# Kernel optimization log

Measured on AMD Instinct MI355X. Metric: run time of the kernel, lower is better.

## Reference

```python
import jax, jax.numpy as jnp
import numpy as np

N = 30000      # nodes
E = 400000     # edges per sparse set / GAT graph
F_IN = 512     # num_features
NHID = 128     # nhid
H = 4          # GAT heads
NCLS = 10      # num_classes
NSETS = 5      # num_gat = (3**2-1)//2 + 1
EPS = 1e-5     # BatchNorm eps


def setup_inputs() -> dict:
    key = jax.random.key(0)
    ks = jax.random.split(key, 24)
    s_in = 1.0 / np.sqrt(F_IN)
    s_h = 1.0 / np.sqrt(NHID)
    s_hh = 1.0 / np.sqrt(H * NHID)
    inp = {
        "x": jax.random.normal(ks[0], (N, F_IN), jnp.float32),
        "edge_index": jax.random.randint(ks[1], (2, E), 0, N),
        "scatter_idx": jax.random.randint(ks[2], (NSETS, 2, E), 0, N),
        "scatter_w": jax.random.normal(ks[3], (NSETS, E), jnp.float32) * 0.1,
        "lin_in_W": jax.random.normal(ks[4], (F_IN, NHID), jnp.float32) * s_in,
        "lin_in_b": jnp.zeros((NHID,), jnp.float32),
        "gat_W": jax.random.normal(ks[5], (NSETS, NHID, H * NHID), jnp.float32) * s_h,
        "att_src": jax.random.normal(ks[6], (NSETS, H, NHID), jnp.float32) * s_h,
        "att_dst": jax.random.normal(ks[7], (NSETS, H, NHID), jnp.float32) * s_h,
        "gat_b": jnp.zeros((NSETS, H * NHID), jnp.float32),
        "mlp_W": jax.random.normal(ks[8], (NSETS, H * NHID, NHID), jnp.float32) * s_hh,
        "mlp_b": jnp.zeros((NSETS, NHID), jnp.float32),
        "bn_g": jnp.ones((NSETS, NHID), jnp.float32),
        "bn_b": jnp.zeros((NSETS, NHID), jnp.float32),
        "bn_m": jax.random.normal(ks[9], (NSETS, NHID), jnp.float32) * 0.1,
        "bn_v": jax.random.uniform(ks[10], (NSETS, NHID), jnp.float32) + 0.5,
        "bn0_g": jnp.ones((NHID,), jnp.float32),
        "bn0_b": jnp.zeros((NHID,), jnp.float32),
        "bn0_m": jax.random.normal(ks[11], (NHID,), jnp.float32) * 0.1,
        "bn0_v": jax.random.uniform(ks[12], (NHID,), jnp.float32) + 0.5,
        "out_W": jax.random.normal(ks[13], (NHID, NCLS), jnp.float32) * s_h,
        "out_b": jnp.zeros((NCLS,), jnp.float32),
    }
    return inp


def _forward(x, edge_index, scatter_idx, scatter_w, lin_in_W, lin_in_b,
             gat_W, att_src, att_dst, gat_b, mlp_W, mlp_b,
             bn_g, bn_b, bn_m, bn_v, bn0_g, bn0_b, bn0_m, bn0_v, out_W, out_b):
    # solo_pass: gather source features, weight by edge value, scatter-add at dest
    def sp(i, xx):
        msg = scatter_w[i][:, None] * xx[scatter_idx[i, 0]]          # [E, NHID]
        return jax.ops.segment_sum(msg, scatter_idx[i, 1], num_segments=N)

    h = x @ lin_in_W + lin_in_b                                       # [N, NHID]
    x0 = sp(0, h)
    xhs = [jnp.abs(sp(i, h)) for i in range(1, NSETS)]
    xs = [x0] + [sp(0, xh) for xh in xhs]

    # GATConv adds self-loops by default
    loops = jnp.arange(N)
    src = jnp.concatenate([edge_index[0], loops])
    dst = jnp.concatenate([edge_index[1], loops])

    def gat(i, xx):
        hh = (xx @ gat_W[i]).reshape(N, H, NHID)                      # [N,H,C]
        a_s = (hh * att_src[i]).sum(-1)                               # [N,H]
        a_d = (hh * att_dst[i]).sum(-1)                               # [N,H]
        e = jax.nn.leaky_relu(a_s[src] + a_d[dst], 0.2)               # [E+N,H]
        m = jax.ops.segment_max(e, dst, num_segments=N)
        ex = jnp.exp(e - m[dst])
        den = jax.ops.segment_sum(ex, dst, num_segments=N)
        alpha = ex / (den[dst] + 1e-16)                               # [E+N,H]
        out = jax.ops.segment_sum(alpha[:, :, None] * hh[src], dst, num_segments=N)
        return out.reshape(N, H * NHID) + gat_b[i]

    # Seq(ELU, Dropout(eval=no-op), Linear, BatchNorm1d(eval))
    def mlp(i, xx):
        z = jax.nn.elu(xx) @ mlp_W[i] + mlp_b[i]
        return (z - bn_m[i]) * jax.lax.rsqrt(bn_v[i] + EPS) * bn_g[i] + bn_b[i]

    outs = [mlp(i, gat(i, xs[i])) for i in range(NSETS)]
    x_stage2 = h + outs[0] + outs[1] + outs[2] + outs[3] + outs[4]

    z = (x_stage2 - bn0_m) * jax.lax.rsqrt(bn0_v + EPS) * bn0_g + bn0_b
    z = jax.nn.elu(z) @ out_W + out_b
    return jax.nn.log_softmax(z, axis=1)


def reference(x, edge_index, scatter_idx, scatter_w, lin_in_W, lin_in_b,
              gat_W, att_src, att_dst, gat_b, mlp_W, mlp_b,
              bn_g, bn_b, bn_m, bn_v, bn0_g, bn0_b, bn0_m, bn0_v, out_W, out_b):
    return _forward(x, edge_index, scatter_idx, scatter_w, lin_in_W, lin_in_b,
                    gat_W, att_src, att_dst, gat_b, mlp_W, mlp_b,
                    bn_g, bn_b, bn_m, bn_v, bn0_g, bn0_b, bn0_m, bn0_v, out_W, out_b)
```

## Files before the change

### kernel.cpp

```cpp
#include <hip/hip_runtime.h>
#include <cstdint>
#include <cstddef>

#define NN 30000
#define NE 400000
#define EG (NE + NN)
#define NSETS 5
#define NCLS 10
#define BN_EPS 1e-5f

#define NBKT 118
#define CHUNK 4096
#define NWG_SET 98
#define NWG_GAT 105
#define NWGMAX 105
#define NBLK_BIN (5 * NWG_SET + NWG_GAT)
#define NBLK_SORT (6 * NBKT)

typedef __bf16 bf16x8 __attribute__((ext_vector_type(8)));
typedef float  f32x4  __attribute__((ext_vector_type(4)));

constexpr size_t alg(size_t x) { return (x + 255) & ~size_t(255); }
constexpr size_t OFF_U1    = 0;
constexpr size_t OFF_HB    = OFF_U1   + alg((size_t)5 * NN * 128 * 2);
constexpr size_t OFF_X2    = OFF_HB   + alg((size_t)NN * 128 * 2);
constexpr size_t OFF_AGG   = OFF_X2   + alg((size_t)NN * 128 * 4);
constexpr size_t OFF_GOUT  = OFF_AGG  + alg((size_t)NN * 512 * 2);
constexpr size_t OFF_WT    = OFF_GOUT + alg((size_t)NN * 512 * 2);
constexpr size_t OFF_WATT  = OFF_WT   + alg((size_t)11 * 65536 * 2);
constexpr size_t OFF_OFF6  = OFF_WATT + alg((size_t)5 * 2 * 4 * 128 * 4);
constexpr size_t OFF_SPP   = OFF_OFF6 + alg((size_t)6 * (NN + 1) * 4);
constexpr size_t OFF_GSRC  = OFF_SPP  + alg((size_t)NSETS * NE * 8);
constexpr size_t OFF_CNT   = OFF_GSRC + alg((size_t)EG * 4);
constexpr size_t OFF_AS5   = OFF_CNT  + alg((size_t)12 * NN * 4);
constexpr size_t OFF_AD5   = OFF_AS5  + alg((size_t)5 * NN * 4 * 4);
constexpr size_t WS_NEED   = OFF_AD5  + alg((size_t)5 * NN * 4 * 4);

__device__ __forceinline__ float lrelu02(float v) { return v > 0.f ? v : 0.2f * v; }
__device__ __forceinline__ float eluf(float v)    { return v > 0.f ? v : __expf(v) - 1.f; }
__device__ __forceinline__ float bf2f(unsigned u) {
    union { unsigned i; float f; } c; c.i = u << 16; return c.f;
}
__device__ __forceinline__ unsigned short f2bf(float f) {
    union { float f; unsigned i; } c; c.f = f;
    unsigned u = c.i + 0x7FFFu + ((c.i >> 16) & 1u);
    return (unsigned short)(u >> 16);
}
__device__ __forceinline__ void gload_lds16(const void* g, void* l) {
    __builtin_amdgcn_global_load_lds(
        (const __attribute__((address_space(1))) void*)(uintptr_t)g,
        (__attribute__((address_space(3))) void*)(unsigned)(uintptr_t)l,
        16, 0, 0);
}

__device__ __forceinline__ void chunk_map(int blk, int& g, int& wg, int& e0, int& e1) {
    if (blk < 5 * NWG_SET) { g = blk / NWG_SET; wg = blk - g * NWG_SET; }
    else                   { g = 5;             wg = blk - 5 * NWG_SET; }
    e0 = wg * CHUNK;
    e1 = min(e0 + CHUNK, (g < 5) ? NE : EG);
}

#define PREP_CVX_B 1024
#define PREP_TRW_B 512
#define PREP_WAT_B 20
#define PREP_HIST_B NBLK_BIN
#define PREP_GRID (PREP_CVX_B + PREP_TRW_B + PREP_WAT_B + PREP_HIST_B)

__global__ void prep1(const int* __restrict__ scat_idx, const int* __restrict__ edge_ix,
                      int* __restrict__ bh,
                      const float* __restrict__ x, unsigned short* __restrict__ xb,
                      const float* __restrict__ lin_W, const float* __restrict__ gat_W,
                      const float* __restrict__ mlp_W,
                      unsigned short* __restrict__ linWT, unsigned short* __restrict__ gatWT,
                      unsigned short* __restrict__ mlpWT,
                      const float* __restrict__ att_src, const float* __restrict__ att_dst,
                      float* __restrict__ watt) {
    __shared__ int h[NBKT];
    const int b = blockIdx.x;
    if (b < PREP_CVX_B) {
        const int total = NN * 512 / 4;
        for (int i = b * 256 + threadIdx.x; i < total; i += PREP_CVX_B * 256) {
            float4 v = *(const float4*)(x + (size_t)i * 4);
            ushort4 o;
            o.x = f2bf(v.x); o.y = f2bf(v.y); o.z = f2bf(v.z); o.w = f2bf(v.w);
            *(ushort4*)(xb + (size_t)i * 4) = o;
        }
    } else if (b < PREP_CVX_B + PREP_TRW_B) {
        const int bb = b - PREP_CVX_B;
        const int total = 65536 + 2 * 327680;
        for (int i = bb * 256 + threadIdx.x; i < total; i += PREP_TRW_B * 256) {
            if (i < 65536) {
                int n = i >> 9, k = i & 511;
                linWT[i] = f2bf(lin_W[(size_t)k * 128 + n]);
            } else if (i < 65536 + 327680) {
                int li = i - 65536;
                int st = li >> 16, r = li & 65535;
                int n = r >> 7, k = r & 127;
                gatWT[li] = f2bf(gat_W[(size_t)st * 65536 + (size_t)k * 512 + n]);
            } else {
                int li = i - 65536 - 327680;
                int st = li >> 16, r = li & 65535;
                int n = r >> 9, k = r & 511;
                mlpWT[li] = f2bf(mlp_W[(size_t)st * 65536 + (size_t)k * 128 + n]);
            }
        }
    } else if (b < PREP_CVX_B + PREP_TRW_B + PREP_WAT_B) {
        const int tid = (b - PREP_CVX_B - PREP_TRW_B) * 256 + threadIdx.x;
        if (tid < 5120) {
            int k = tid & 127, hh = (tid >> 7) & 3, tt = (tid >> 9) & 1, i = tid >> 10;
            const float* att = (tt == 0 ? att_src : att_dst) + ((size_t)i * 4 + hh) * 128;
            const float* Wr  = gat_W + ((size_t)i * 128 + k) * 512 + hh * 128;
            float s = 0.f;
            #pragma unroll 8
            for (int c = 0; c < 128; ++c) s = fmaf(Wr[c], att[c], s);
            watt[tid] = s;
        }
    } else {
        const int blk = b - (PREP_CVX_B + PREP_TRW_B + PREP_WAT_B);
        int g, wg, e0, e1;
        chunk_map(blk, g, wg, e0, e1);
        for (int i = threadIdx.x; i < NBKT; i += 256) h[i] = 0;
        __syncthreads();
        if (g < 5) {
            const int* dsts = scat_idx + (size_t)g * 2 * NE + NE;
            for (int e = e0 + threadIdx.x; e < e1; e += 256)
                atomicAdd(&h[dsts[e] >> 8], 1);
        } else {
            for (int e = e0 + threadIdx.x; e < e1; e += 256) {
                int d = (e < NE) ? edge_ix[NE + e] : (e - NE);
                atomicAdd(&h[d >> 8], 1);
            }
        }
        __syncthreads();
        for (int i = threadIdx.x; i < NBKT; i += 256)
            bh[(size_t)(g * NBKT + i) * NWGMAX + wg] = h[i];
    }
}

__global__ void bktscan(const int* __restrict__ bh, int* __restrict__ bb, int* __restrict__ off6) {
    const int g = blockIdx.x;
    const int t = threadIdx.x;
    const int nwg = (g < 5) ? NWG_SET : NWG_GAT;
    __shared__ int s[128];
    int tot = 0;
    if (t < NBKT) {
        const int* p = bh + (size_t)(g * NBKT + t) * NWGMAX;
        for (int w = 0; w < nwg; ++w) tot += p[w];
    }
    s[t] = tot;
    __syncthreads();
    for (int d = 1; d < 128; d <<= 1) {
        int u = (t >= d) ? s[t - d] : 0;
        __syncthreads();
        s[t] += u;
        __syncthreads();
    }
    if (t < NBKT) bb[g * 132 + t] = s[t] - tot;
    if (t == NBKT - 1) {
        bb[g * 132 + NBKT] = s[t];
        off6[g * (NN + 1) + NN] = s[t];
    }
}

__global__ void wgscan(const int* __restrict__ bb, int* __restrict__ bh) {
    const int gb = blockIdx.x;
    const int g = gb / NBKT, bk = gb - g * NBKT;
    __shared__ int s[128];
    const int t = threadIdx.x;
    const int nwg = (g < 5) ? NWG_SET : NWG_GAT;
    int v = (t < nwg) ? bh[(size_t)gb * NWGMAX + t] : 0;
    s[t] = v;
    __syncthreads();
    for (int d = 1; d < 128; d <<= 1) {
        int u = (t >= d) ? s[t - d] : 0;
        __syncthreads();
        s[t] += u;
        __syncthreads();
    }
    const int base = bb[g * 132 + bk];
    if (t < nwg) bh[(size_t)gb * NWGMAX + t] = base + (s[t] - v);
}

__global__ void __launch_bounds__(256) binP(const int* __restrict__ scat_idx, const float* __restrict__ scat_w,
                                            const int* __restrict__ edge_ix, const int* __restrict__ pos,
                                            int2* __restrict__ stg_sp, int* __restrict__ stg_g) {
    __shared__ int lpos[NBKT];
    __shared__ int lcur[NBKT];
    int g, wg, e0, e1;
    chunk_map(blockIdx.x, g, wg, e0, e1);
    for (int i = threadIdx.x; i < NBKT; i += 256) {
        lpos[i] = pos[(size_t)(g * NBKT + i) * NWGMAX + wg];
        lcur[i] = 0;
    }
    __syncthreads();
    if (g < 5) {
        const int* si = scat_idx + (size_t)g * 2 * NE;
        const float* sw = scat_w + (size_t)g * NE;
        for (int e = e0 + threadIdx.x; e < e1; e += 256) {
            int src = si[e], d = si[NE + e];
            int r = atomicAdd(&lcur[d >> 8], 1);
            int2 pk; pk.x = src | (d << 15); pk.y = __float_as_int(sw[e]);
            stg_sp[(size_t)g * NE + lpos[d >> 8] + r] = pk;
        }
    } else {
        for (int e = e0 + threadIdx.x; e < e1; e += 256) {
            int src, d;
            if (e < NE) { src = edge_ix[e]; d = edge_ix[NE + e]; }
            else        { src = e - NE;     d = src; }
            int r = atomicAdd(&lcur[d >> 8], 1);
            stg_g[lpos[d >> 8] + r] = src | (d << 15);
        }
    }
}

__global__ void __launch_bounds__(256) sortP(const int* __restrict__ bb,
                                             const int2* __restrict__ stg_sp, const int* __restrict__ stg_g,
                                             int2* __restrict__ spp, int* __restrict__ g_src,
                                             int* __restrict__ off6) {
    __shared__ int lcnt[256];
    __shared__ int loff[257];
    const int gb = blockIdx.x;
    const int g = gb / NBKT, bk = gb - g * NBKT;
    const int n0 = bk << 8;
    const int nlen = min(256, NN - n0);
    const int base = bb[g * 132 + bk];
    const int end  = bb[g * 132 + bk + 1];
    const int t = threadIdx.x;
    lcnt[t] = 0;
    __syncthreads();
    if (g < 5) {
        for (int j = base + t; j < end; j += 256)
            atomicAdd(&lcnt[((stg_sp[(size_t)g * NE + j].x >> 15) & 0x7fff) - n0], 1);
    } else {
        for (int j = base + t; j < end; j += 256)
            atomicAdd(&lcnt[((stg_g[j] >> 15) & 0x7fff) - n0], 1);
    }
    __syncthreads();
    int v = lcnt[t];
    __syncthreads();
    for (int d = 1; d < 256; d <<= 1) {
        int u = (t >= d) ? lcnt[t - d] : 0;
        __syncthreads();
        lcnt[t] += u;
        __syncthreads();
    }
    loff[t] = base + lcnt[t] - v;
    if (t == 255) loff[256] = base + lcnt[255];
    __syncthreads();
    if (t < nlen) off6[g * (NN + 1) + n0 + t] = loff[t];
    lcnt[t] = 0;
    __syncthreads();
    if (g < 5) {
        for (int j = base + t; j < end; j += 256) {
            int2 pk = stg_sp[(size_t)g * NE + j];
            int ln = ((pk.x >> 15) & 0x7fff) - n0;
            int p = loff[ln] + atomicAdd(&lcnt[ln], 1);
            int2 o; o.x = pk.x & 0x7fff; o.y = pk.y;
            spp[(size_t)g * NE + p] = o;
        }
    } else {
        for (int j = base + t; j < end; j += 256) {
            int w = stg_g[j];
            int ln = ((w >> 15) & 0x7fff) - n0;
            int p = loff[ln] + atomicAdd(&lcnt[ln], 1);
            g_src[p] = w & 0x7fff;
        }
    }
}

template<int ROWS>
__device__ __forceinline__ void stage64(const unsigned short* __restrict__ src, int ld,
                                        int row0, int maxrow, int k0, char* lds, int t) {
    const int wave = t >> 6, lane = t & 63;
    const int sub = lane >> 3;
    const int kch = (lane & 7) ^ sub;
    for (int j = wave; j < ROWS / 8; j += 4) {
        int grow = row0 + j * 8 + sub;
        if (grow > maxrow) grow = maxrow;
        gload_lds16(src + (size_t)grow * ld + k0 + kch * 8, lds + j * 1024);
    }
}

__global__ void __launch_bounds__(256) mgemm_lin(const unsigned short* __restrict__ A,
                                                 const unsigned short* __restrict__ BT,
                                                 const float* __restrict__ bias,
                                                 unsigned short* __restrict__ outb,
                                                 float* __restrict__ x2) {
    constexpr int K = 512, NC = 128;
    __shared__ __align__(16) char As[64 * 128];
    __shared__ __align__(16) char Bs[128 * 128];
    const int t = threadIdx.x, wave = t >> 6, lane = t & 63;
    const int bm = blockIdx.x * 64;
    const int wr = (wave >> 1) * 32, wc = (wave & 1) * 64;
    const int l15 = lane & 15, l4 = lane >> 4;
    const int rsw = (l15 & 7) << 4;
    f32x4 acc[2][4] = {};

    for (int kt = 0; kt < K; kt += 64) {
        stage64<64>(A, K, bm, NN - 1, kt, As, t);
        stage64<128>(BT, K, 0, NC - 1, kt, Bs, t);
        __syncthreads();
        #pragma unroll
        for (int kk = 0; kk < 2; ++kk) {
            bf16x8 af[2], bf[4];
            const int koff = kk * 64 + l4 * 16;
            #pragma unroll
            for (int fm = 0; fm < 2; ++fm)
                af[fm] = *(const bf16x8*)(As + (wr + fm * 16 + l15) * 128 + (koff ^ rsw));
            #pragma unroll
            for (int fn = 0; fn < 4; ++fn)
                bf[fn] = *(const bf16x8*)(Bs + (wc + fn * 16 + l15) * 128 + (koff ^ rsw));
            #pragma unroll
            for (int fm = 0; fm < 2; ++fm)
                #pragma unroll
                for (int fn = 0; fn < 4; ++fn)
                    acc[fm][fn] = __builtin_amdgcn_mfma_f32_16x16x32_bf16(af[fm], bf[fn], acc[fm][fn], 0, 0, 0);
        }
        __syncthreads();
    }

    #pragma unroll
    for (int fn = 0; fn < 4; ++fn) {
        const int c = wc + fn * 16 + l15;
        const float bias_c = bias[c];
        #pragma unroll
        for (int fm = 0; fm < 2; ++fm) {
            #pragma unroll
            for (int rg = 0; rg < 4; ++rg) {
                int r = bm + wr + fm * 16 + l4 * 4 + rg;
                if (r < NN) {
                    float v = acc[fm][fn][rg] + bias_c;
                    outb[(size_t)r * NC + c] = f2bf(v);
                    x2[(size_t)r * NC + c] = v;
                }
            }
        }
    }
}

__global__ void __launch_bounds__(256) fusedGM(const unsigned short* __restrict__ agg,
                                               const unsigned short* __restrict__ gatWT,
                                               const unsigned short* __restrict__ mlpWT,
                                               const float* __restrict__ gat_b,
                                               const float* __restrict__ mlp_b,
                                               const float* __restrict__ bng, const float* __restrict__ bnb,
                                               const float* __restrict__ bnm, const float* __restrict__ bnv,
                                               float* __restrict__ x2) {
    __shared__ __align__(16) char U[49152];
    __shared__ __align__(16) char gtile[16384];
    const int t = threadIdx.x, wave = t >> 6, lane = t & 63;
    const int bm = blockIdx.x * 64;
    const int wr = (wave >> 1) * 32, wc = (wave & 1) * 64;
    const int l15 = lane & 15, l4 = lane >> 4;
    const int rsw = (l15 & 7) << 4;
    f32x4 acc2[2][4] = {};

    #pragma unroll
    for (int h = 0; h < 4; ++h) {
        stage64<64>(agg, 512, bm, NN - 1, h * 128,       U,         t);
        stage64<64>(agg, 512, bm, NN - 1, h * 128 + 64,  U + 8192,  t);
        stage64<128>(gatWT, 128, h * 128, 511, 0,        U + 16384, t);
        stage64<128>(gatWT, 128, h * 128, 511, 64,       U + 32768, t);
        __syncthreads();

        f32x4 a1[2][4] = {};
        #pragma unroll
        for (int ks = 0; ks < 4; ++ks) {
            const char* Asb = U + (ks >> 1) * 8192;
            const char* Bsb = U + 16384 + (ks >> 1) * 16384;
            const int koff = (ks & 1) * 64 + l4 * 16;
            bf16x8 af[2], bf[4];
            #pragma unroll
            for (int fm = 0; fm < 2; ++fm)
                af[fm] = *(const bf16x8*)(Asb + (wr + fm * 16 + l15) * 128 + (koff ^ rsw));
            #pragma unroll
            for (int fn = 0; fn < 4; ++fn)
                bf[fn] = *(const bf16x8*)(Bsb + (wc + fn * 16 + l15) * 128 + (koff ^ rsw));
            #pragma unroll
            for (int fm = 0; fm < 2; ++fm)
                #pragma unroll
                for (int fn = 0; fn < 4; ++fn)
                    a1[fm][fn] = __builtin_amdgcn_mfma_f32_16x16x32_bf16(af[fm], bf[fn], a1[fm][fn], 0, 0, 0);
        }
        __syncthreads();

        #pragma unroll
        for (int fn = 0; fn < 4; ++fn) {
            const int cc = wc + fn * 16 + l15;
            const float gb = gat_b[h * 128 + cc];
            #pragma unroll
            for (int fm = 0; fm < 2; ++fm) {
                #pragma unroll
                for (int rg = 0; rg < 4; ++rg) {
                    const int r = wr + fm * 16 + l4 * 4 + rg;
                    const unsigned short v = f2bf(eluf(a1[fm][fn][rg] + gb));
                    *(unsigned short*)(gtile + r * 256 + ((((cc >> 3) ^ (r & 7)) << 4) | ((cc & 7) << 1))) = v;
                }
            }
        }
        stage64<128>(mlpWT, 512, 0, 127, h * 128,      U,         t);
        stage64<128>(mlpWT, 512, 0, 127, h * 128 + 64, U + 16384, t);
        __syncthreads();

        #pragma unroll
        for (int ks = 0; ks < 4; ++ks) {
            const int s2 = ks >> 1, kk = ks & 1;
            const char* slab = U + s2 * 16384;
            bf16x8 af[2], bf[4];
            #pragma unroll
            for (int fm = 0; fm < 2; ++fm) {
                const int r2 = wr + fm * 16 + l15;
                const int chunk = (s2 * 8 + kk * 4 + l4) ^ (r2 & 7);
                af[fm] = *(const bf16x8*)(gtile + r2 * 256 + (chunk << 4));
            }
            const int koff = kk * 64 + l4 * 16;
            #pragma unroll
            for (int fn = 0; fn < 4; ++fn)
                bf[fn] = *(const bf16x8*)(slab + (wc + fn * 16 + l15) * 128 + (koff ^ rsw));
            #pragma unroll
            for (int fm = 0; fm < 2; ++fm)
                #pragma unroll
                for (int fn = 0; fn < 4; ++fn)
                    acc2[fm][fn] = __builtin_amdgcn_mfma_f32_16x16x32_bf16(af[fm], bf[fn], acc2[fm][fn], 0, 0, 0);
        }
        __syncthreads();
    }

    #pragma unroll
    for (int fn = 0; fn < 4; ++fn) {
        const int c = wc + fn * 16 + l15;
        const float sc = bng[c] * rsqrtf(bnv[c] + BN_EPS);
        const float sh = bnb[c] - bnm[c] * sc;
        const float mb = mlp_b[c];
        #pragma unroll
        for (int fm = 0; fm < 2; ++fm) {
            #pragma unroll
            for (int rg = 0; rg < 4; ++rg) {
                int r = bm + wr + fm * 16 + l4 * 4 + rg;
                if (r < NN)
                    x2[(size_t)r * 128 + c] += (acc2[fm][fn][rg] + mb) * sc + sh;
            }
        }
    }
}

__global__ void __launch_bounds__(256) sp_abs_all(const int* __restrict__ off6,
                                                  const int2* __restrict__ spp,
                                                  const unsigned short* __restrict__ hb,
                                                  unsigned short* __restrict__ tmpI) {
    const int wid  = blockIdx.x * 4 + (threadIdx.x >> 6);
    const int lane = threadIdx.x & 63;
    const int co   = lane * 2;
    float a[4][2];
    #pragma unroll
    for (int y = 0; y < 4; ++y) {
        const int* off = off6 + (y + 1) * (NN + 1);
        const int2* pk = spp + (size_t)(y + 1) * NE;
        const int s0 = off[wid], s1 = off[wid + 1];
        float a0 = 0.f, a1 = 0.f;
        int j = s0;
        for (; j + 3 < s1; j += 4) {
            int2 e0 = pk[j], e1 = pk[j + 1], e2 = pk[j + 2], e3 = pk[j + 3];
            unsigned v0 = *(const unsigned*)(hb + (size_t)e0.x * 128 + co);
            unsigned v1 = *(const unsigned*)(hb + (size_t)e1.x * 128 + co);
            unsigned v2 = *(const unsigned*)(hb + (size_t)e2.x * 128 + co);
            unsigned v3 = *(const unsigned*)(hb + (size_t)e3.x * 128 + co);
            float w0 = __int_as_float(e0.y), w1 = __int_as_float(e1.y);
            float w2 = __int_as_float(e2.y), w3 = __int_as_float(e3.y);
            a0 = fmaf(w0, bf2f(v0 & 0xffffu), a0); a1 = fmaf(w0, bf2f(v0 >> 16), a1);
            a0 = fmaf(w1, bf2f(v1 & 0xffffu), a0); a1 = fmaf(w1, bf2f(v1 >> 16), a1);
            a0 = fmaf(w2, bf2f(v2 & 0xffffu), a0); a1 = fmaf(w2, bf2f(v2 >> 16), a1);
            a0 = fmaf(w3, bf2f(v3 & 0xffffu), a0); a1 = fmaf(w3, bf2f(v3 >> 16), a1);
        }
        for (; j < s1; ++j) {
            int2 e = pk[j];
            float wj = __int_as_float(e.y);
            unsigned v = *(const unsigned*)(hb + (size_t)e.x * 128 + co);
            a0 = fmaf(wj, bf2f(v & 0xffffu), a0);
            a1 = fmaf(wj, bf2f(v >> 16), a1);
        }
        a[y][0] = fabsf(a0);
        a[y][1] = fabsf(a1);
    }
    uint4 o;
    o.x = (unsigned)f2bf(a[0][0]) | ((unsigned)f2bf(a[1][0]) << 16);
    o.y = (unsigned)f2bf(a[2][0]) | ((unsigned)f2bf(a[3][0]) << 16);
    o.z = (unsigned)f2bf(a[0][1]) | ((unsigned)f2bf(a[1][1]) << 16);
    o.w = (unsigned)f2bf(a[2][1]) | ((unsigned)f2bf(a[3][1]) << 16);
    *(uint4*)(tmpI + (size_t)wid * 512 + co * 4) = o;
}

__global__ void __launch_bounds__(256) sp_fused5(const int* __restrict__ off0,
                                                 const int2* __restrict__ spp0,
                                                 const unsigned short* __restrict__ hb,
                                                 const unsigned short* __restrict__ tmpI,
                                                 unsigned short* __restrict__ xcur5,
                                                 const float* __restrict__ watt,
                                                 float* __restrict__ as5,
                                                 float* __restrict__ ad5) {
    __shared__ float sWatt[5120];
    for (int i = threadIdx.x; i < 5120; i += 256) sWatt[i] = watt[i];
    __syncthreads();

    const int wid  = blockIdx.x * 4 + (threadIdx.x >> 6);
    const int lane = threadIdx.x & 63;
    const int co   = lane * 2;
    const int s0 = off0[wid], s1 = off0[wid + 1];

    float a[5][2] = {};
    int j = s0;
    for (; j + 3 < s1; j += 4) {
        int2 e0 = spp0[j], e1 = spp0[j + 1], e2 = spp0[j + 2], e3 = spp0[j + 3];
        unsigned h0 = *(const unsigned*)(hb + (size_t)e0.x * 128 + co);
        unsigned h1 = *(const unsigned*)(hb + (size_t)e1.x * 128 + co);
        unsigned h2 = *(const unsigned*)(hb + (size_t)e2.x * 128 + co);
        unsigned h3 = *(const unsigned*)(hb + (size_t)e3.x * 128 + co);
        uint4 t0 = *(const uint4*)(tmpI + (size_t)e0.x * 512 + co * 4);
        uint4 t1 = *(const uint4*)(tmpI + (size_t)e1.x * 512 + co * 4);
        uint4 t2 = *(const uint4*)(tmpI + (size_t)e2.x * 512 + co * 4);
        uint4 t3 = *(const uint4*)(tmpI + (size_t)e3.x * 512 + co * 4);
        float w0 = __int_as_float(e0.y), w1 = __int_as_float(e1.y);
        float w2 = __int_as_float(e2.y), w3 = __int_as_float(e3.y);
        #define ACC1(W, H, T) \
            a[0][0] = fmaf(W, bf2f((H) & 0xffffu), a[0][0]); a[0][1] = fmaf(W, bf2f((H) >> 16), a[0][1]); \
            a[1][0] = fmaf(W, bf2f((T).x & 0xffffu), a[1][0]); a[2][0] = fmaf(W, bf2f((T).x >> 16), a[2][0]); \
            a[3][0] = fmaf(W, bf2f((T).y & 0xffffu), a[3][0]); a[4][0] = fmaf(W, bf2f((T).y >> 16), a[4][0]); \
            a[1][1] = fmaf(W, bf2f((T).z & 0xffffu), a[1][1]); a[2][1] = fmaf(W, bf2f((T).z >> 16), a[2][1]); \
            a[3][1] = fmaf(W, bf2f((T).w & 0xffffu), a[3][1]); a[4][1] = fmaf(W, bf2f((T).w >> 16), a[4][1]);
        ACC1(w0, h0, t0)
        ACC1(w1, h1, t1)
        ACC1(w2, h2, t2)
        ACC1(w3, h3, t3)
    }
    for (; j < s1; ++j) {
        int2 e = spp0[j];
        float wj = __int_as_float(e.y);
        unsigned hh = *(const unsigned*)(hb + (size_t)e.x * 128 + co);
        uint4 tt = *(const uint4*)(tmpI + (size_t)e.x * 512 + co * 4);
        ACC1(wj, hh, tt)
    }
    #undef ACC1
    #pragma unroll
    for (int y = 0; y < 5; ++y) {
        unsigned o = (unsigned)f2bf(a[y][0]) | ((unsigned)f2bf(a[y][1]) << 16);
        *(unsigned*)(xcur5 + (size_t)y * NN * 128 + (size_t)wid * 128 + co) = o;
    }

    #pragma unroll
    for (int i = 0; i < 5; ++i) {
        #pragma unroll
        for (int h = 0; h < 4; ++h) {
            const float* wS = sWatt + ((i * 2 + 0) * 4 + h) * 128;
            const float* wD = sWatt + ((i * 2 + 1) * 4 + h) * 128;
            float ps = a[i][0] * wS[co] + a[i][1] * wS[co + 1];
            float pd = a[i][0] * wD[co] + a[i][1] * wD[co + 1];
            #pragma unroll
            for (int dd = 1; dd < 64; dd <<= 1) { ps += __shfl_xor(ps, dd); pd += __shfl_xor(pd, dd); }
            if (lane == 0) {
                as5[(size_t)i * NN * 4 + (size_t)wid * 4 + h] = ps;
                ad5[(size_t)i * NN * 4 + (size_t)wid * 4 + h] = pd;
            }
        }
    }
}

__device__ __forceinline__ void acc8(float* a, float al, uint4 v) {
    a[0] = fmaf(al, bf2f(v.x & 0xffffu), a[0]); a[1] = fmaf(al, bf2f(v.x >> 16), a[1]);
    a[2] = fmaf(al, bf2f(v.y & 0xffffu), a[2]); a[3] = fmaf(al, bf2f(v.y >> 16), a[3]);
    a[4] = fmaf(al, bf2f(v.z & 0xffffu), a[4]); a[5] = fmaf(al, bf2f(v.z >> 16), a[5]);
    a[6] = fmaf(al, bf2f(v.w & 0xffffu), a[6]); a[7] = fmaf(al, bf2f(v.w >> 16), a[7]);
}

__global__ void __launch_bounds__(256) gat_agg2(const int* __restrict__ goff, const int* __restrict__ gsrc,
                                                const float* __restrict__ as_, const float* __restrict__ ad_,
                                                const unsigned short* __restrict__ xcur,
                                                unsigned short* __restrict__ agg) {
    const int wid  = blockIdx.x * 4 + (threadIdx.x >> 6);
    const int lane = threadIdx.x & 63;
    const int hd   = lane >> 4;
    const int cl   = (lane & 15) * 8;
    const int s0 = goff[wid], s1 = goff[wid + 1];
    const float4 adv4 = *(const float4*)(ad_ + (size_t)wid * 4);

    float m[4] = {-1e30f, -1e30f, -1e30f, -1e30f};
    float s[4] = {0.f, 0.f, 0.f, 0.f};
    for (int j = s0 + lane; j < s1; j += 64) {
        const int si = gsrc[j];
        float4 av = *(const float4*)(as_ + (size_t)si * 4);
        float e[4] = {lrelu02(av.x + adv4.x), lrelu02(av.y + adv4.y),
                      lrelu02(av.z + adv4.z), lrelu02(av.w + adv4.w)};
        #pragma unroll
        for (int h = 0; h < 4; ++h) {
            if (e[h] > m[h]) { s[h] = s[h] * __expf(m[h] - e[h]) + 1.f; m[h] = e[h]; }
            else             { s[h] += __expf(e[h] - m[h]); }
        }
    }
    #pragma unroll
    for (int d = 1; d < 64; d <<= 1) {
        #pragma unroll
        for (int h = 0; h < 4; ++h) {
            float om = __shfl_xor(m[h], d);
            float os = __shfl_xor(s[h], d);
            float nm = fmaxf(m[h], om);
            s[h] = s[h] * __expf(m[h] - nm) + os * __expf(om - nm);
            m[h] = nm;
        }
    }
    const float advh = hd == 0 ? adv4.x : hd == 1 ? adv4.y : hd == 2 ? adv4.z : adv4.w;
    const float mv   = hd == 0 ? m[0]   : hd == 1 ? m[1]   : hd == 2 ? m[2]   : m[3];
    const float dv   = hd == 0 ? s[0]   : hd == 1 ? s[1]   : hd == 2 ? s[2]   : s[3];
    const float inv  = 1.f / (dv + 1e-16f);

    float ac[8] = {};
    int j = s0;
    for (; j + 3 < s1; j += 4) {
        int i0 = gsrc[j], i1 = gsrc[j + 1], i2 = gsrc[j + 2], i3 = gsrc[j + 3];
        float q0 = as_[(size_t)i0 * 4 + hd], q1 = as_[(size_t)i1 * 4 + hd];
        float q2 = as_[(size_t)i2 * 4 + hd], q3 = as_[(size_t)i3 * 4 + hd];
        uint4 v0 = *(const uint4*)(xcur + (size_t)i0 * 128 + cl);
        uint4 v1 = *(const uint4*)(xcur + (size_t)i1 * 128 + cl);
        uint4 v2 = *(const uint4*)(xcur + (size_t)i2 * 128 + cl);
        uint4 v3 = *(const uint4*)(xcur + (size_t)i3 * 128 + cl);
        float al0 = __expf(lrelu02(q0 + advh) - mv) * inv;
        float al1 = __expf(lrelu02(q1 + advh) - mv) * inv;
        float al2 = __expf(lrelu02(q2 + advh) - mv) * inv;
        float al3 = __expf(lrelu02(q3 + advh) - mv) * inv;
        acc8(ac, al0, v0); acc8(ac, al1, v1); acc8(ac, al2, v2); acc8(ac, al3, v3);
    }
    for (; j < s1; ++j) {
        int si = gsrc[j];
        float q = as_[(size_t)si * 4 + hd];
        uint4 v = *(const uint4*)(xcur + (size_t)si * 128 + cl);
        float al = __expf(lrelu02(q + advh) - mv) * inv;
        acc8(ac, al, v);
    }
    uint4 ov;
    ov.x = (unsigned)f2bf(ac[0]) | ((unsigned)f2bf(ac[1]) << 16);
    ov.y = (unsigned)f2bf(ac[2]) | ((unsigned)f2bf(ac[3]) << 16);
    ov.z = (unsigned)f2bf(ac[4]) | ((unsigned)f2bf(ac[5]) << 16);
    ov.w = (unsigned)f2bf(ac[6]) | ((unsigned)f2bf(ac[7]) << 16);
    *(uint4*)(agg + (size_t)wid * 512 + hd * 128 + cl) = ov;
}

__global__ void __launch_bounds__(256) final_out(const float* __restrict__ x2,
                                                 const float* __restrict__ bn0g, const float* __restrict__ bn0b,
                                                 const float* __restrict__ bn0m, const float* __restrict__ bn0v,
                                                 const float* __restrict__ outW, const float* __restrict__ outb,
                                                 float* __restrict__ out) {
    __shared__ float sW[128 * 12];
    __shared__ float sSc[128], sSh[128];
    for (int i = threadIdx.x; i < 1280; i += 256) {
        int r = i / 10, c = i - r * 10;
        sW[r * 12 + c] = outW[i];
    }
    if (threadIdx.x < 128) {
        int c = threadIdx.x;
        float sc = bn0g[c] * rsqrtf(bn0v[c] + BN_EPS);
        sSc[c] = sc;
        sSh[c] = bn0b[c] - bn0m[c] * sc;
    }
    __syncthreads();
    const int wid  = blockIdx.x * 4 + (threadIdx.x >> 6);
    const int lane = threadIdx.x & 63;
    const int c0 = lane * 2;
    float2 a = *(const float2*)(x2 + (size_t)wid * 128 + c0);
    float a0 = eluf(a.x * sSc[c0] + sSh[c0]);
    float a1 = eluf(a.y * sSc[c0 + 1] + sSh[c0 + 1]);
    float p[NCLS];
    #pragma unroll
    for (int j = 0; j < NCLS; ++j)
        p[j] = a0 * sW[c0 * 12 + j] + a1 * sW[(c0 + 1) * 12 + j];
    #pragma unroll
    for (int j = 0; j < NCLS; ++j) {
        float v = p[j];
        v += __shfl_xor(v, 1);  v += __shfl_xor(v, 2);  v += __shfl_xor(v, 4);
        v += __shfl_xor(v, 8);  v += __shfl_xor(v, 16); v += __shfl_xor(v, 32);
        p[j] = v;
    }
    float z[NCLS];
    #pragma unroll
    for (int j = 0; j < NCLS; ++j) z[j] = p[j] + outb[j];
    float m = z[0];
    #pragma unroll
    for (int j = 1; j < NCLS; ++j) m = fmaxf(m, z[j]);
    float ssum = 0.f;
    #pragma unroll
    for (int j = 0; j < NCLS; ++j) ssum += __expf(z[j] - m);
    float lse = m + __logf(ssum);
    #pragma unroll
    for (int j = 0; j < NCLS; ++j)
        if (lane == j) out[(size_t)wid * NCLS + j] = z[j] - lse;
}

extern "C" void kernel_launch(void* const* d_in, const int* in_sizes, int n_in,
                              void* d_out, int out_size, void* d_ws, size_t ws_size,
                              hipStream_t stream) {
    const float* x        = (const float*)d_in[0];
    const int*   edge_ix  = (const int*)  d_in[1];
    const int*   scat_idx = (const int*)  d_in[2];
    const float* scat_w   = (const float*)d_in[3];
    const float* lin_W    = (const float*)d_in[4];
    const float* lin_b    = (const float*)d_in[5];
    const float* gat_W    = (const float*)d_in[6];
    const float* att_src  = (const float*)d_in[7];
    const float* att_dst  = (const float*)d_in[8];
    const float* gat_b    = (const float*)d_in[9];
    const float* mlp_W    = (const float*)d_in[10];
    const float* mlp_b    = (const float*)d_in[11];
    const float* bn_g     = (const float*)d_in[12];
    const float* bn_b     = (const float*)d_in[13];
    const float* bn_m     = (const float*)d_in[14];
    const float* bn_v     = (const float*)d_in[15];
    const float* bn0_g    = (const float*)d_in[16];
    const float* bn0_b    = (const float*)d_in[17];
    const float* bn0_m    = (const float*)d_in[18];
    const float* bn0_v    = (const float*)d_in[19];
    const float* out_W    = (const float*)d_in[20];
    const float* out_b    = (const float*)d_in[21];
    float* out = (float*)d_out;

    char* ws = (char*)d_ws;
    unsigned short* xb    = (unsigned short*)(ws + OFF_U1);
    unsigned short* xcur5 = (unsigned short*)(ws + OFF_U1);
    unsigned short* hb    = (unsigned short*)(ws + OFF_HB);
    float*          x2    = (float*)(ws + OFF_X2);
    unsigned short* agg   = (unsigned short*)(ws + OFF_AGG);
    unsigned short* tmpI  = (unsigned short*)(ws + OFF_GOUT);
    int2*  stg_sp = (int2*)(ws + OFF_GOUT);
    int*   stg_g  = (int*)(ws + OFF_GOUT + (size_t)NSETS * NE * 8);
    unsigned short* wt    = (unsigned short*)(ws + OFF_WT);
    unsigned short* linWT = wt;
    unsigned short* gatWT = wt + 65536;
    unsigned short* mlpWT = wt + 65536 * 6;
    float* watt   = (float*)(ws + OFF_WATT);
    int*   off6   = (int*)(ws + OFF_OFF6);
    int2*  spp    = (int2*)(ws + OFF_SPP);
    int*   g_src  = (int*)(ws + OFF_GSRC);
    int*   bh     = (int*)(ws + OFF_CNT);
    int*   bb     = bh + NBLK_SORT * NWGMAX;
    float* as5    = (float*)(ws + OFF_AS5);
    float* ad5    = (float*)(ws + OFF_AD5);

    const dim3 b256(256);

    prep1<<<PREP_GRID, b256, 0, stream>>>(scat_idx, edge_ix, bh, x, xb,
                                          lin_W, gat_W, mlp_W, linWT, gatWT, mlpWT,
                                          att_src, att_dst, watt);
    bktscan<<<6, 128, 0, stream>>>(bh, bb, off6);
    wgscan<<<NBLK_SORT, 128, 0, stream>>>(bb, bh);
    binP<<<NBLK_BIN, b256, 0, stream>>>(scat_idx, scat_w, edge_ix, bh, stg_sp, stg_g);
    sortP<<<NBLK_SORT, b256, 0, stream>>>(bb, stg_sp, stg_g, spp, g_src, off6);

    mgemm_lin<<<469, b256, 0, stream>>>(xb, linWT, lin_b, hb, x2);

    sp_abs_all<<<7500, b256, 0, stream>>>(off6, spp, hb, tmpI);
    sp_fused5<<<7500, b256, 0, stream>>>(off6, spp, hb, tmpI, xcur5, watt, as5, ad5);

    for (int i = 0; i < NSETS; ++i) {
        gat_agg2<<<7500, b256, 0, stream>>>(off6 + 5 * (NN + 1), g_src,
                                            as5 + (size_t)i * NN * 4, ad5 + (size_t)i * NN * 4,
                                            xcur5 + (size_t)i * NN * 128, agg);
        fusedGM<<<469, b256, 0, stream>>>(agg, gatWT + (size_t)i * 65536, mlpWT + (size_t)i * 65536,
                                          gat_b + (size_t)i * 512, mlp_b + (size_t)i * 128,
                                          bn_g + (size_t)i * 128, bn_b + (size_t)i * 128,
                                          bn_m + (size_t)i * 128, bn_v + (size_t)i * 128, x2);
    }

    final_out<<<7500, b256, 0, stream>>>(x2, bn0_g, bn0_b, bn0_m, bn0_v, out_W, out_b, out);
}
```

Baseline: 679.4 us.

## Precompute softmax max and inverse denominators for all five GAT sets in one kernel

Adds a kernel, att_mden5, that computes the per-destination attention max and inverse softmax denominator for all five GAT sets in a single pass over the edges, using a two-pass max-then-sum instead of an online softmax. Each gat_agg2 launch then reads these from a workspace buffer instead of recomputing them with an edge sweep and shuffle reductions. The edge-gather loops in sp_abs_all and sp_fused5 are also unrolled from 4 to 8 so more loads are in flight. The cost is an extra launch, a new workspace buffer, and higher register pressure in the new kernel, which holds 40 accumulators per lane.

```diff
diff --git a/kernel.cpp b/kernel.cpp
--- a/kernel.cpp
+++ b/kernel.cpp
@@ -34,7 +34,8 @@
 constexpr size_t OFF_CNT   = OFF_GSRC + alg((size_t)EG * 4);
 constexpr size_t OFF_AS5   = OFF_CNT  + alg((size_t)12 * NN * 4);
 constexpr size_t OFF_AD5   = OFF_AS5  + alg((size_t)5 * NN * 4 * 4);
-constexpr size_t WS_NEED   = OFF_AD5  + alg((size_t)5 * NN * 4 * 4);
+constexpr size_t OFF_MVI   = OFF_AD5  + alg((size_t)5 * NN * 4 * 4);
+constexpr size_t WS_NEED   = OFF_MVI  + alg((size_t)5 * NN * 8 * 4);
 
 __device__ __forceinline__ float lrelu02(float v) { return v > 0.f ? v : 0.2f * v; }
 __device__ __forceinline__ float eluf(float v)    { return v > 0.f ? v : __expf(v) - 1.f; }
@@ -459,18 +460,19 @@
         const int s0 = off[wid], s1 = off[wid + 1];
         float a0 = 0.f, a1 = 0.f;
         int j = s0;
-        for (; j + 3 < s1; j += 4) {
-            int2 e0 = pk[j], e1 = pk[j + 1], e2 = pk[j + 2], e3 = pk[j + 3];
-            unsigned v0 = *(const unsigned*)(hb + (size_t)e0.x * 128 + co);
-            unsigned v1 = *(const unsigned*)(hb + (size_t)e1.x * 128 + co);
-            unsigned v2 = *(const unsigned*)(hb + (size_t)e2.x * 128 + co);
-            unsigned v3 = *(const unsigned*)(hb + (size_t)e3.x * 128 + co);
-            float w0 = __int_as_float(e0.y), w1 = __int_as_float(e1.y);
-            float w2 = __int_as_float(e2.y), w3 = __int_as_float(e3.y);
-            a0 = fmaf(w0, bf2f(v0 & 0xffffu), a0); a1 = fmaf(w0, bf2f(v0 >> 16), a1);
-            a0 = fmaf(w1, bf2f(v1 & 0xffffu), a0); a1 = fmaf(w1, bf2f(v1 >> 16), a1);
-            a0 = fmaf(w2, bf2f(v2 & 0xffffu), a0); a1 = fmaf(w2, bf2f(v2 >> 16), a1);
-            a0 = fmaf(w3, bf2f(v3 & 0xffffu), a0); a1 = fmaf(w3, bf2f(v3 >> 16), a1);
+        for (; j + 7 < s1; j += 8) {
+            int2 e[8];
+            unsigned v[8];
+            #pragma unroll
+            for (int q = 0; q < 8; ++q) e[q] = pk[j + q];
+            #pragma unroll
+            for (int q = 0; q < 8; ++q) v[q] = *(const unsigned*)(hb + (size_t)e[q].x * 128 + co);
+            #pragma unroll
+            for (int q = 0; q < 8; ++q) {
+                float w = __int_as_float(e[q].y);
+                a0 = fmaf(w, bf2f(v[q] & 0xffffu), a0);
+                a1 = fmaf(w, bf2f(v[q] >> 16), a1);
+            }
         }
         for (; j < s1; ++j) {
             int2 e = pk[j];
@@ -508,29 +510,29 @@
     const int s0 = off0[wid], s1 = off0[wid + 1];
 
     float a[5][2] = {};
+    #define ACC1(W, H, T) \
+        a[0][0] = fmaf(W, bf2f((H) & 0xffffu), a[0][0]); a[0][1] = fmaf(W, bf2f((H) >> 16), a[0][1]); \
+        a[1][0] = fmaf(W, bf2f((T).x & 0xffffu), a[1][0]); a[2][0] = fmaf(W, bf2f((T).x >> 16), a[2][0]); \
+        a[3][0] = fmaf(W, bf2f((T).y & 0xffffu), a[3][0]); a[4][0] = fmaf(W, bf2f((T).y >> 16), a[4][0]); \
+        a[1][1] = fmaf(W, bf2f((T).z & 0xffffu), a[1][1]); a[2][1] = fmaf(W, bf2f((T).z >> 16), a[2][1]); \
+        a[3][1] = fmaf(W, bf2f((T).w & 0xffffu), a[3][1]); a[4][1] = fmaf(W, bf2f((T).w >> 16), a[4][1]);
     int j = s0;
-    for (; j + 3 < s1; j += 4) {
-        int2 e0 = spp0[j], e1 = spp0[j + 1], e2 = spp0[j + 2], e3 = spp0[j + 3];
-        unsigned h0 = *(const unsigned*)(hb + (size_t)e0.x * 128 + co);
-        unsigned h1 = *(const unsigned*)(hb + (size_t)e1.x * 128 + co);
-        unsigned h2 = *(const unsigned*)(hb + (size_t)e2.x * 128 + co);
-        unsigned h3 = *(const unsigned*)(hb + (size_t)e3.x * 128 + co);
-        uint4 t0 = *(const uint4*)(tmpI + (size_t)e0.x * 512 + co * 4);
-        uint4 t1 = *(const uint4*)(tmpI + (size_t)e1.x * 512 + co * 4);
-        uint4 t2 = *(const uint4*)(tmpI + (size_t)e2.x * 512 + co * 4);
-        uint4 t3 = *(const uint4*)(tmpI + (size_t)e3.x * 512 + co * 4);
-        float w0 = __int_as_float(e0.y), w1 = __int_as_float(e1.y);
-        float w2 = __int_as_float(e2.y), w3 = __int_as_float(e3.y);
-        #define ACC1(W, H, T) \
-            a[0][0] = fmaf(W, bf2f((H) & 0xffffu), a[0][0]); a[0][1] = fmaf(W, bf2f((H) >> 16), a[0][1]); \
-            a[1][0] = fmaf(W, bf2f((T).x & 0xffffu), a[1][0]); a[2][0] = fmaf(W, bf2f((T).x >> 16), a[2][0]); \
-            a[3][0] = fmaf(W, bf2f((T).y & 0xffffu), a[3][0]); a[4][0] = fmaf(W, bf2f((T).y >> 16), a[4][0]); \
-            a[1][1] = fmaf(W, bf2f((T).z & 0xffffu), a[1][1]); a[2][1] = fmaf(W, bf2f((T).z >> 16), a[2][1]); \
-            a[3][1] = fmaf(W, bf2f((T).w & 0xffffu), a[3][1]); a[4][1] = fmaf(W, bf2f((T).w >> 16), a[4][1]);
-        ACC1(w0, h0, t0)
-        ACC1(w1, h1, t1)
-        ACC1(w2, h2, t2)
-        ACC1(w3, h3, t3)
+    for (; j + 7 < s1; j += 8) {
+        int2 e[8];
+        #pragma unroll
+        for (int q = 0; q < 8; ++q) e[q] = spp0[j + q];
+        unsigned hv[8];
+        uint4 tv[8];
+        #pragma unroll
+        for (int q = 0; q < 8; ++q) {
+            hv[q] = *(const unsigned*)(hb + (size_t)e[q].x * 128 + co);
+            tv[q] = *(const uint4*)(tmpI + (size_t)e[q].x * 512 + co * 4);
+        }
+        #pragma unroll
+        for (int q = 0; q < 8; ++q) {
+            float w = __int_as_float(e[q].y);
+            ACC1(w, hv[q], tv[q])
+        }
     }
     for (; j < s1; ++j) {
         int2 e = spp0[j];
@@ -564,6 +566,75 @@
     }
 }
 
+__global__ void __launch_bounds__(256) att_mden5(const int* __restrict__ goff, const int* __restrict__ gsrc,
+                                                 const float* __restrict__ as5, const float* __restrict__ ad5,
+                                                 float* __restrict__ mvi) {
+    const int wid  = blockIdx.x * 4 + (threadIdx.x >> 6);
+    const int lane = threadIdx.x & 63;
+    const int s0 = goff[wid], s1 = goff[wid + 1];
+    float4 adv[5];
+    #pragma unroll
+    for (int i = 0; i < 5; ++i)
+        adv[i] = *(const float4*)(ad5 + (size_t)i * NN * 4 + (size_t)wid * 4);
+
+    float m[5][4];
+    #pragma unroll
+    for (int i = 0; i < 5; ++i)
+        #pragma unroll
+        for (int h = 0; h < 4; ++h) m[i][h] = -1e30f;
+    for (int j = s0 + lane; j < s1; j += 64) {
+        const int si = gsrc[j];
+        float4 av[5];
+        #pragma unroll
+        for (int i = 0; i < 5; ++i)
+            av[i] = *(const float4*)(as5 + (size_t)i * NN * 4 + (size_t)si * 4);
+        #pragma unroll
+        for (int i = 0; i < 5; ++i)
+            #pragma unroll
+            for (int h = 0; h < 4; ++h)
+                m[i][h] = fmaxf(m[i][h], lrelu02((&av[i].x)[h] + (&adv[i].x)[h]));
+    }
+    #pragma unroll
+    for (int d = 1; d < 64; d <<= 1)
+        #pragma unroll
+        for (int i = 0; i < 5; ++i)
+            #pragma unroll
+            for (int h = 0; h < 4; ++h)
+                m[i][h] = fmaxf(m[i][h], __shfl_xor(m[i][h], d));
+
+    float s[5][4] = {};
+    for (int j = s0 + lane; j < s1; j += 64) {
+        const int si = gsrc[j];
+        float4 av[5];
+        #pragma unroll
+        for (int i = 0; i < 5; ++i)
+            av[i] = *(const float4*)(as5 + (size_t)i * NN * 4 + (size_t)si * 4);
+        #pragma unroll
+        for (int i = 0; i < 5; ++i)
+            #pragma unroll
+            for (int h = 0; h < 4; ++h)
+                s[i][h] += __expf(lrelu02((&av[i].x)[h] + (&adv[i].x)[h]) - m[i][h]);
+    }
+    #pragma unroll
+    for (int d = 1; d < 64; d <<= 1)
+        #pragma unroll
+        for (int i = 0; i < 5; ++i)
+            #pragma unroll
+            for (int h = 0; h < 4; ++h)
+                s[i][h] += __shfl_xor(s[i][h], d);
+
+    if (lane == 0) {
+        #pragma unroll
+        for (int i = 0; i < 5; ++i) {
+            float4 mv = {m[i][0], m[i][1], m[i][2], m[i][3]};
+            float4 iv = {1.f / (s[i][0] + 1e-16f), 1.f / (s[i][1] + 1e-16f),
+                         1.f / (s[i][2] + 1e-16f), 1.f / (s[i][3] + 1e-16f)};
+            *(float4*)(mvi + (size_t)i * NN * 8 + (size_t)wid * 8)     = mv;
+            *(float4*)(mvi + (size_t)i * NN * 8 + (size_t)wid * 8 + 4) = iv;
+        }
+    }
+}
+
 __device__ __forceinline__ void acc8(float* a, float al, uint4 v) {
     a[0] = fmaf(al, bf2f(v.x & 0xffffu), a[0]); a[1] = fmaf(al, bf2f(v.x >> 16), a[1]);
     a[2] = fmaf(al, bf2f(v.y & 0xffffu), a[2]); a[3] = fmaf(al, bf2f(v.y >> 16), a[3]);
@@ -573,6 +644,7 @@
 
 __global__ void __launch_bounds__(256) gat_agg2(const int* __restrict__ goff, const int* __restrict__ gsrc,
                                                 const float* __restrict__ as_, const float* __restrict__ ad_,
+                                                const float* __restrict__ mvi,
                                                 const unsigned short* __restrict__ xcur,
                                                 unsigned short* __restrict__ agg) {
     const int wid  = blockIdx.x * 4 + (threadIdx.x >> 6);
@@ -581,35 +653,11 @@
     const int cl   = (lane & 15) * 8;
     const int s0 = goff[wid], s1 = goff[wid + 1];
     const float4 adv4 = *(const float4*)(ad_ + (size_t)wid * 4);
-
-    float m[4] = {-1e30f, -1e30f, -1e30f, -1e30f};
-    float s[4] = {0.f, 0.f, 0.f, 0.f};
-    for (int j = s0 + lane; j < s1; j += 64) {
-        const int si = gsrc[j];
-        float4 av = *(const float4*)(as_ + (size_t)si * 4);
-        float e[4] = {lrelu02(av.x + adv4.x), lrelu02(av.y + adv4.y),
-                      lrelu02(av.z + adv4.z), lrelu02(av.w + adv4.w)};
-        #pragma unroll
-        for (int h = 0; h < 4; ++h) {
-            if (e[h] > m[h]) { s[h] = s[h] * __expf(m[h] - e[h]) + 1.f; m[h] = e[h]; }
-            else             { s[h] += __expf(e[h] - m[h]); }
-        }
-    }
-    #pragma unroll
-    for (int d = 1; d < 64; d <<= 1) {
-        #pragma unroll
-        for (int h = 0; h < 4; ++h) {
-            float om = __shfl_xor(m[h], d);
-            float os = __shfl_xor(s[h], d);
-            float nm = fmaxf(m[h], om);
-            s[h] = s[h] * __expf(m[h] - nm) + os * __expf(om - nm);
-            m[h] = nm;
-        }
-    }
-    const float advh = hd == 0 ? adv4.x : hd == 1 ? adv4.y : hd == 2 ? adv4.z : adv4.w;
-    const float mv   = hd == 0 ? m[0]   : hd == 1 ? m[1]   : hd == 2 ? m[2]   : m[3];
-    const float dv   = hd == 0 ? s[0]   : hd == 1 ? s[1]   : hd == 2 ? s[2]   : s[3];
-    const float inv  = 1.f / (dv + 1e-16f);
+    const float4 mv4  = *(const float4*)(mvi + (size_t)wid * 8);
+    const float4 iv4  = *(const float4*)(mvi + (size_t)wid * 8 + 4);
+    const float advh = (&adv4.x)[hd];
+    const float mv   = (&mv4.x)[hd];
+    const float inv  = (&iv4.x)[hd];
 
     float ac[8] = {};
     int j = s0;
@@ -740,6 +788,7 @@
     int*   bb     = bh + NBLK_SORT * NWGMAX;
     float* as5    = (float*)(ws + OFF_AS5);
     float* ad5    = (float*)(ws + OFF_AD5);
+    float* mvi    = (float*)(ws + OFF_MVI);
 
     const dim3 b256(256);
 
@@ -756,9 +805,12 @@
     sp_abs_all<<<7500, b256, 0, stream>>>(off6, spp, hb, tmpI);
     sp_fused5<<<7500, b256, 0, stream>>>(off6, spp, hb, tmpI, xcur5, watt, as5, ad5);
 
+    att_mden5<<<7500, b256, 0, stream>>>(off6 + 5 * (NN + 1), g_src, as5, ad5, mvi);
+
     for (int i = 0; i < NSETS; ++i) {
         gat_agg2<<<7500, b256, 0, stream>>>(off6 + 5 * (NN + 1), g_src,
                                             as5 + (size_t)i * NN * 4, ad5 + (size_t)i * NN * 4,
+                                            mvi + (size_t)i * NN * 8,
                                             xcur5 + (size_t)i * NN * 128, agg);
         fusedGM<<<469, b256, 0, stream>>>(agg, gatWT + (size_t)i * 65536, mlpWT + (size_t)i * 65536,
                                           gat_b + (size_t)i * 512, mlp_b + (size_t)i * 128,
```

Result: slower. 743.7 us (+9.5%).
